# Performance work log

Hardware: AMD Instinct MI355X
Metric: run time of the kernel (lower is better)

The kernel has to match this reference:

```python
import jax, jax.numpy as jnp
import numpy as np

B, N, K = 128, 131072, 256


def setup_inputs() -> dict:
    key = jax.random.key(0)
    k1, k2 = jax.random.split(key)
    score = jax.random.normal(k1, (B, N), dtype=jnp.float32)
    roi = jax.random.uniform(k2, (B, N, 4), dtype=jnp.float32)
    return {"score": score, "roi": roi, "k": K}


def reference(score, roi, k):
    # top-k over the anchor dim, sorted descending (matches tf.nn.top_k sorted=True)
    top_k_score, top_k_index = jax.lax.top_k(score, k)  # [B, k], [B, k]
    # gather ROI rows: equivalent of tf.gather_nd with (batch_idx, anchor_idx)
    roi_selected = jnp.take_along_axis(roi, top_k_index[:, :, None], axis=1)  # [B, k, 4]
    return roi_selected, top_k_score
```

## Files before the change

### kernel.cpp

```cpp
#include <hip/hip_runtime.h>
#include <stdint.h>


#define BATCH   128
#define NANCH   131072
#define KSEL    256
#define SPLITS  8
#define CHUNK   (NANCH / SPLITS)
#define TPB     256
#define V4PT    (CHUNK / TPB / 4)
#define NBUCK   4096
#define CAPMAX  8192
#define SORTCAP 2048

typedef unsigned long long ull;

__device__ __forceinline__ unsigned ord_of(float f) {
    unsigned u = __float_as_uint(f);
    return (u & 0x80000000u) ? ~u : (u | 0x80000000u);
}
__device__ __forceinline__ float f_of_ord(unsigned o) {
    unsigned u = (o & 0x80000000u) ? (o ^ 0x80000000u) : ~o;
    return __uint_as_float(u);
}

__global__ __launch_bounds__(TPB) void topk_stage1(
    const float* __restrict__ score, ull* __restrict__ cand,
    int* __restrict__ cnt, int cap)
{
    __shared__ int hist[NBUCK];
    __shared__ int scan[TPB];
    __shared__ int s_bstar;
    __shared__ int s_base;

    const int t  = threadIdx.x;
    const int sp = blockIdx.x;
    const int b  = blockIdx.y;

    const float4* src = (const float4*)(score + (size_t)b * NANCH + (size_t)sp * CHUNK);
    float4 v[V4PT];
#pragma unroll
    for (int i = 0; i < V4PT; ++i) v[i] = src[i * TPB + t];

    for (int i = t; i < NBUCK; i += TPB) hist[i] = 0;
    __syncthreads();

#pragma unroll
    for (int i = 0; i < V4PT; ++i) {
        atomicAdd(&hist[ord_of(v[i].x) >> 20], 1);
        atomicAdd(&hist[ord_of(v[i].y) >> 20], 1);
        atomicAdd(&hist[ord_of(v[i].z) >> 20], 1);
        atomicAdd(&hist[ord_of(v[i].w) >> 20], 1);
    }
    __syncthreads();

    int ps = 0;
#pragma unroll
    for (int p = 0; p < 16; ++p) ps += hist[t * 16 + p];
    scan[t] = ps;
    __syncthreads();
    for (int off = 1; off < TPB; off <<= 1) {
        int add = (t + off < TPB) ? scan[t + off] : 0;
        __syncthreads();
        scan[t] += add;
        __syncthreads();
    }
    {
        int running = (t + 1 < TPB) ? scan[t + 1] : 0;
#pragma unroll
        for (int p = 15; p >= 0; --p) {
            int nr = running + hist[t * 16 + p];
            if (nr >= KSEL && running < KSEL) s_bstar = t * 16 + p;
            running = nr;
        }
    }
    __syncthreads();
    const unsigned thr = (unsigned)s_bstar << 20;

    int qc = 0;
#pragma unroll
    for (int i = 0; i < V4PT; ++i) {
        qc += (ord_of(v[i].x) >= thr);
        qc += (ord_of(v[i].y) >= thr);
        qc += (ord_of(v[i].z) >= thr);
        qc += (ord_of(v[i].w) >= thr);
    }
    __syncthreads();
    scan[t] = qc;
    __syncthreads();
    for (int off = 1; off < TPB; off <<= 1) {
        int add = (t >= off) ? scan[t - off] : 0;
        __syncthreads();
        scan[t] += add;
        __syncthreads();
    }
    if (t == TPB - 1) s_base = atomicAdd(&cnt[b], scan[TPB - 1]);
    __syncthreads();

    int pos = s_base + scan[t] - qc;
    ull* cb = cand + (size_t)b * cap;
    const int nbase = sp * CHUNK;
#pragma unroll
    for (int i = 0; i < V4PT; ++i) {
        const int n0 = nbase + 4 * (i * TPB + t);
        unsigned o;
        o = ord_of(v[i].x);
        if (o >= thr && pos < cap) { cb[pos++] = ((ull)o << 32) | (unsigned)(NANCH - 1 - n0); }
        o = ord_of(v[i].y);
        if (o >= thr && pos < cap) { cb[pos++] = ((ull)o << 32) | (unsigned)(NANCH - 2 - n0); }
        o = ord_of(v[i].z);
        if (o >= thr && pos < cap) { cb[pos++] = ((ull)o << 32) | (unsigned)(NANCH - 3 - n0); }
        o = ord_of(v[i].w);
        if (o >= thr && pos < cap) { cb[pos++] = ((ull)o << 32) | (unsigned)(NANCH - 4 - n0); }
    }
}

__global__ __launch_bounds__(TPB) void topk_stage2(
    const ull* __restrict__ cand, const int* __restrict__ cnt,
    const float* __restrict__ roi, float* __restrict__ out_roi,
    float* __restrict__ out_score, int cap)
{
    __shared__ int hist[NBUCK];
    __shared__ int scan[TPB];
    __shared__ ull buf[SORTCAP];
    __shared__ int s_bstar, s_csel;

    const int t = threadIdx.x;
    const int b = blockIdx.x;
    const int c = min(cnt[b], cap);
    const ull* cb = cand + (size_t)b * cap;

    for (int i = t; i < NBUCK; i += TPB) hist[i] = 0;
    if (t == 0) s_csel = 0;
    __syncthreads();
    for (int i = t; i < c; i += TPB) atomicAdd(&hist[(unsigned)(cb[i] >> 52)], 1);
    __syncthreads();

    int ps = 0;
#pragma unroll
    for (int p = 0; p < 16; ++p) ps += hist[t * 16 + p];
    scan[t] = ps;
    __syncthreads();
    for (int off = 1; off < TPB; off <<= 1) {
        int add = (t + off < TPB) ? scan[t + off] : 0;
        __syncthreads();
        scan[t] += add;
        __syncthreads();
    }
    {
        int running = (t + 1 < TPB) ? scan[t + 1] : 0;
#pragma unroll
        for (int p = 15; p >= 0; --p) {
            int nr = running + hist[t * 16 + p];
            if (nr >= KSEL && running < KSEL) s_bstar = t * 16 + p;
            running = nr;
        }
    }
    __syncthreads();
    const unsigned bstar = (unsigned)s_bstar;

    for (int i = t; i < c; i += TPB) {
        ull k = cb[i];
        if ((unsigned)(k >> 52) >= bstar) {
            int p = atomicAdd(&s_csel, 1);
            if (p < SORTCAP) buf[p] = k;
        }
    }
    __syncthreads();
    const int C = min(s_csel, SORTCAP);
    int P = KSEL;
    while (P < C) P <<= 1;
    for (int i = C + t; i < P; i += TPB) buf[i] = 0;
    __syncthreads();

    for (int kk = 2; kk <= P; kk <<= 1) {
        for (int j = kk >> 1; j > 0; j >>= 1) {
            for (int i = t; i < P; i += TPB) {
                int ixj = i ^ j;
                if (ixj > i) {
                    ull a = buf[i], d = buf[ixj];
                    bool up = (i & kk) == 0;
                    bool sw = up ? (a < d) : (a > d);
                    if (sw) { buf[i] = d; buf[ixj] = a; }
                }
            }
            __syncthreads();
        }
    }

    ull k = buf[t];
    unsigned o = (unsigned)(k >> 32);
    int idx = NANCH - 1 - (int)(unsigned)(k & 0xffffffffull);
    out_score[b * KSEL + t] = f_of_ord(o);
    float4 r = ((const float4*)roi)[(size_t)b * NANCH + idx];
    ((float4*)out_roi)[b * KSEL + t] = r;
}

extern "C" void kernel_launch(void* const* d_in, const int* in_sizes, int n_in,
                              void* d_out, int out_size, void* d_ws, size_t ws_size,
                              hipStream_t stream)
{
    const float* score = (const float*)d_in[0];
    const float* roi   = (const float*)d_in[1];
    float* out_roi   = (float*)d_out;
    float* out_score = (float*)d_out + (size_t)BATCH * KSEL * 4;

    int* cnt  = (int*)d_ws;
    ull* cand = (ull*)((char*)d_ws + 4096);
    long long avail = ((long long)ws_size - 4096) / (long long)(sizeof(ull) * BATCH);
    int cap = (int)avail;
    if (cap > CAPMAX) cap = CAPMAX;
    if (cap < 1) cap = 1;

    hipMemsetAsync(cnt, 0, BATCH * sizeof(int), stream);
    topk_stage1<<<dim3(SPLITS, BATCH), TPB, 0, stream>>>(score, cand, cnt, cap);
    topk_stage2<<<BATCH, TPB, 0, stream>>>(cand, cnt, roi, out_roi, out_score, cap);
}
```

Baseline: 370.4 us.

## Use wave-shuffle scans and a 512-thread register-cached second stage

Replaces the barrier-heavy shared-memory Hillis-Steele scans in both stages with wave-level shuffle prefix/suffix scans plus a small per-wave totals combine, cutting the number of __syncthreads. Stage 2 now runs with 512 threads, loads the candidate keys into registers once instead of reading global memory twice, and splits the output writes so ROI gathers and score writes go to different threads. The risk is higher register pressure from the per-thread key array in stage 2, and the change relies on a 64-wide wavefront.

New measurement: 360.3 us. 1.03x faster.

```diff
diff --git a/kernel.cpp b/kernel.cpp
--- a/kernel.cpp
+++ b/kernel.cpp
@@ -12,6 +12,8 @@
 #define NBUCK   4096
 #define CAPMAX  8192
 #define SORTCAP 2048
+#define TPB2    512
+#define RPT2    (CAPMAX / TPB2)
 
 typedef unsigned long long ull;
 
@@ -22,6 +24,23 @@
 __device__ __forceinline__ float f_of_ord(unsigned o) {
     unsigned u = (o & 0x80000000u) ? (o ^ 0x80000000u) : ~o;
     return __uint_as_float(u);
+}
+
+__device__ __forceinline__ int wave_incl_prefix(int v, int lane) {
+#pragma unroll
+    for (int off = 1; off < 64; off <<= 1) {
+        int n = __shfl_up(v, off);
+        if (lane >= off) v += n;
+    }
+    return v;
+}
+__device__ __forceinline__ int wave_incl_suffix(int v, int lane) {
+#pragma unroll
+    for (int off = 1; off < 64; off <<= 1) {
+        int n = __shfl_down(v, off);
+        if (lane + off < 64) v += n;
+    }
+    return v;
 }
 
 __global__ __launch_bounds__(TPB) void topk_stage1(
@@ -29,13 +48,15 @@
     int* __restrict__ cnt, int cap)
 {
     __shared__ int hist[NBUCK];
-    __shared__ int scan[TPB];
+    __shared__ int wtot[TPB / 64];
     __shared__ int s_bstar;
     __shared__ int s_base;
 
-    const int t  = threadIdx.x;
-    const int sp = blockIdx.x;
-    const int b  = blockIdx.y;
+    const int t    = threadIdx.x;
+    const int lane = t & 63;
+    const int wid  = t >> 6;
+    const int sp   = blockIdx.x;
+    const int b    = blockIdx.y;
 
     const float4* src = (const float4*)(score + (size_t)b * NANCH + (size_t)sp * CHUNK);
     float4 v[V4PT];
@@ -57,16 +78,16 @@
     int ps = 0;
 #pragma unroll
     for (int p = 0; p < 16; ++p) ps += hist[t * 16 + p];
-    scan[t] = ps;
-    __syncthreads();
-    for (int off = 1; off < TPB; off <<= 1) {
-        int add = (t + off < TPB) ? scan[t + off] : 0;
-        __syncthreads();
-        scan[t] += add;
-        __syncthreads();
-    }
+    int sfx = wave_incl_suffix(ps, lane);
+    if (lane == 0) wtot[wid] = sfx;
+    __syncthreads();
+    int hi = 0;
+#pragma unroll
+    for (int w = 0; w < TPB / 64; ++w) if (w > wid) hi += wtot[w];
+    const int sinc = sfx + hi;
+
     {
-        int running = (t + 1 < TPB) ? scan[t + 1] : 0;
+        int running = sinc - ps;
 #pragma unroll
         for (int p = 15; p >= 0; --p) {
             int nr = running + hist[t * 16 + p];
@@ -85,19 +106,19 @@
         qc += (ord_of(v[i].z) >= thr);
         qc += (ord_of(v[i].w) >= thr);
     }
-    __syncthreads();
-    scan[t] = qc;
-    __syncthreads();
-    for (int off = 1; off < TPB; off <<= 1) {
-        int add = (t >= off) ? scan[t - off] : 0;
-        __syncthreads();
-        scan[t] += add;
-        __syncthreads();
-    }
-    if (t == TPB - 1) s_base = atomicAdd(&cnt[b], scan[TPB - 1]);
-    __syncthreads();
-
-    int pos = s_base + scan[t] - qc;
+    int pfx = wave_incl_prefix(qc, lane);
+    if (lane == 63) wtot[wid] = pfx;
+    __syncthreads();
+    int lo = 0, total = 0;
+#pragma unroll
+    for (int w = 0; w < TPB / 64; ++w) {
+        total += wtot[w];
+        if (w < wid) lo += wtot[w];
+    }
+    if (t == 0) s_base = atomicAdd(&cnt[b], total);
+    __syncthreads();
+
+    int pos = s_base + lo + pfx - qc;
     ull* cb = cand + (size_t)b * cap;
     const int nbase = sp * CHUNK;
 #pragma unroll
@@ -115,67 +136,79 @@
     }
 }
 
-__global__ __launch_bounds__(TPB) void topk_stage2(
+__global__ __launch_bounds__(TPB2) void topk_stage2(
     const ull* __restrict__ cand, const int* __restrict__ cnt,
     const float* __restrict__ roi, float* __restrict__ out_roi,
     float* __restrict__ out_score, int cap)
 {
     __shared__ int hist[NBUCK];
-    __shared__ int scan[TPB];
+    __shared__ int wtot[TPB2 / 64];
     __shared__ ull buf[SORTCAP];
     __shared__ int s_bstar, s_csel;
 
-    const int t = threadIdx.x;
-    const int b = blockIdx.x;
-    const int c = min(cnt[b], cap);
-    const ull* cb = cand + (size_t)b * cap;
-
-    for (int i = t; i < NBUCK; i += TPB) hist[i] = 0;
+    const int t    = threadIdx.x;
+    const int lane = t & 63;
+    const int wid  = t >> 6;
+    const int b    = blockIdx.x;
+    const int c    = min(cnt[b], cap);
+    const ull* cb  = cand + (size_t)b * cap;
+
+    ull rk[RPT2];
+#pragma unroll
+    for (int q = 0; q < RPT2; ++q) {
+        const int i = t + q * TPB2;
+        rk[q] = (i < c) ? cb[i] : 0;
+    }
+
+    for (int i = t; i < NBUCK; i += TPB2) hist[i] = 0;
     if (t == 0) s_csel = 0;
     __syncthreads();
-    for (int i = t; i < c; i += TPB) atomicAdd(&hist[(unsigned)(cb[i] >> 52)], 1);
-    __syncthreads();
-
+#pragma unroll
+    for (int q = 0; q < RPT2; ++q) {
+        if (t + q * TPB2 < c) atomicAdd(&hist[(unsigned)(rk[q] >> 52)], 1);
+    }
+    __syncthreads();
+
+    const int G = NBUCK / TPB2;
     int ps = 0;
 #pragma unroll
-    for (int p = 0; p < 16; ++p) ps += hist[t * 16 + p];
-    scan[t] = ps;
-    __syncthreads();
-    for (int off = 1; off < TPB; off <<= 1) {
-        int add = (t + off < TPB) ? scan[t + off] : 0;
-        __syncthreads();
-        scan[t] += add;
-        __syncthreads();
-    }
+    for (int p = 0; p < G; ++p) ps += hist[t * G + p];
+    int sfx = wave_incl_suffix(ps, lane);
+    if (lane == 0) wtot[wid] = sfx;
+    __syncthreads();
+    int hi = 0;
+#pragma unroll
+    for (int w = 0; w < TPB2 / 64; ++w) if (w > wid) hi += wtot[w];
+    const int sinc = sfx + hi;
     {
-        int running = (t + 1 < TPB) ? scan[t + 1] : 0;
-#pragma unroll
-        for (int p = 15; p >= 0; --p) {
-            int nr = running + hist[t * 16 + p];
-            if (nr >= KSEL && running < KSEL) s_bstar = t * 16 + p;
+        int running = sinc - ps;
+#pragma unroll
+        for (int p = G - 1; p >= 0; --p) {
+            int nr = running + hist[t * G + p];
+            if (nr >= KSEL && running < KSEL) s_bstar = t * G + p;
             running = nr;
         }
     }
     __syncthreads();
     const unsigned bstar = (unsigned)s_bstar;
 
-    for (int i = t; i < c; i += TPB) {
-        ull k = cb[i];
-        if ((unsigned)(k >> 52) >= bstar) {
+#pragma unroll
+    for (int q = 0; q < RPT2; ++q) {
+        if (t + q * TPB2 < c && (unsigned)(rk[q] >> 52) >= bstar) {
             int p = atomicAdd(&s_csel, 1);
-            if (p < SORTCAP) buf[p] = k;
+            if (p < SORTCAP) buf[p] = rk[q];
         }
     }
     __syncthreads();
     const int C = min(s_csel, SORTCAP);
     int P = KSEL;
     while (P < C) P <<= 1;
-    for (int i = C + t; i < P; i += TPB) buf[i] = 0;
+    for (int i = C + t; i < P; i += TPB2) buf[i] = 0;
     __syncthreads();
 
     for (int kk = 2; kk <= P; kk <<= 1) {
         for (int j = kk >> 1; j > 0; j >>= 1) {
-            for (int i = t; i < P; i += TPB) {
+            for (int i = t; i < P; i += TPB2) {
                 int ixj = i ^ j;
                 if (ixj > i) {
                     ull a = buf[i], d = buf[ixj];
@@ -188,12 +221,16 @@
         }
     }
 
-    ull k = buf[t];
-    unsigned o = (unsigned)(k >> 32);
-    int idx = NANCH - 1 - (int)(unsigned)(k & 0xffffffffull);
-    out_score[b * KSEL + t] = f_of_ord(o);
-    float4 r = ((const float4*)roi)[(size_t)b * NANCH + idx];
-    ((float4*)out_roi)[b * KSEL + t] = r;
+    if (t < KSEL) {
+        ull k = buf[t];
+        int idx = NANCH - 1 - (int)(unsigned)(k & 0xffffffffull);
+        float4 r = ((const float4*)roi)[(size_t)b * NANCH + idx];
+        ((float4*)out_roi)[b * KSEL + t] = r;
+    } else if (t < 2 * KSEL) {
+        const int tt = t - KSEL;
+        ull k = buf[tt];
+        out_score[b * KSEL + tt] = f_of_ord((unsigned)(k >> 32));
+    }
 }
 
 extern "C" void kernel_launch(void* const* d_in, const int* in_sizes, int n_in,
@@ -214,5 +251,5 @@
 
     hipMemsetAsync(cnt, 0, BATCH * sizeof(int), stream);
     topk_stage1<<<dim3(SPLITS, BATCH), TPB, 0, stream>>>(score, cand, cnt, cap);
-    topk_stage2<<<BATCH, TPB, 0, stream>>>(cand, cnt, roi, out_roi, out_score, cap);
-}
+    topk_stage2<<<BATCH, TPB2, 0, stream>>>(cand, cnt, roi, out_roi, out_score, cap);
+}
```
